# Kernel optimization log

Hardware: AMD Instinct MI355X
Metric: run time of the kernel (lower is better)

The kernel has to match this reference:

```python
import jax, jax.numpy as jnp
import numpy as np

B, S, D = 2, 2048, 1024
H, HD = 16, 64          # num_heads, head_dim = D // H
W = 31                  # window_size (odd)
E = 1024                # embed_dim


def setup_inputs() -> dict:
    key = jax.random.key(0)
    ks = jax.random.split(key, 12)
    sd = 1.0 / np.sqrt(D)
    so = 1.0 / np.sqrt(H * HD)
    return {
        "x": jax.random.normal(ks[0], (B, S, D), jnp.float32),
        "fsq": jax.random.normal(ks[1], (1, S, D), jnp.float32),   # feature_squeeze_token
        "pos": jax.random.normal(ks[2], (1, S, D), jnp.float32),   # position_token
        "Wq": jax.random.normal(ks[3], (H, D, HD), jnp.float32) * sd,
        "bq": jax.random.normal(ks[4], (H, HD), jnp.float32) * sd,
        "Wk": jax.random.normal(ks[5], (H, D, HD), jnp.float32) * sd,
        "bk": jax.random.normal(ks[6], (H, HD), jnp.float32) * sd,
        "Wv": jax.random.normal(ks[7], (H, D, HD), jnp.float32) * sd,
        "bv": jax.random.normal(ks[8], (H, HD), jnp.float32) * sd,
        "Wo": jax.random.normal(ks[9], (H * HD, E), jnp.float32) * so,
        "bo": jax.random.normal(ks[10], (E,), jnp.float32) * so,
    }


def reference(x, fsq, pos, Wq, bq, Wk, bk, Wv, bv, Wo, bo):
    b, s, d = x.shape
    pad = (W - 1) // 2
    # sliding windows: (B, S, W, D), zero-padded at sequence edges
    xp = jnp.pad(x, ((0, 0), (pad, pad), (0, 0)))
    idx = jnp.arange(s)[:, None] + jnp.arange(W)[None, :]  # (S, W)
    win = xp[:, idx, :]  # (B, S, W, D)
    a = jnp.broadcast_to(fsq[:, :, None, :], (b, s, 1, d))  # squeeze token per pos
    bt = jnp.broadcast_to(pos[:, :, None, :], (b, s, 1, d))  # position token per pos
    kv = jnp.concatenate([win, bt, a], axis=2)  # (B, S, K=W+2, D)
    q = jnp.broadcast_to(fsq, (b, s, d))        # query = squeeze token
    # per-head projections (heads stacked on axis h)
    qh = jnp.einsum("bsd,hde->bhse", q, Wq) + bq[None, :, None, :]        # (B,H,S,HD)
    kh = jnp.einsum("bskd,hde->bhske", kv, Wk) + bk[None, :, None, None, :]
    vh = jnp.einsum("bskd,hde->bhske", kv, Wv) + bv[None, :, None, None, :]
    scores = jnp.einsum("bhse,bhske->bhsk", qh, kh) / jnp.sqrt(jnp.asarray(HD, x.dtype))
    attn = jax.nn.softmax(scores, axis=-1)  # dropout is identity in eval
    outh = jnp.einsum("bhsk,bhske->bhse", attn, vh)  # (B,H,S,HD)
    concat = outh.transpose(0, 2, 1, 3).reshape(b, s, H * HD)  # heads concat order 0..H-1
    return concat @ Wo + bo  # (B, S, E)
```

## Files before the change

### kernel.cpp

```cpp
#include <hip/hip_runtime.h>


typedef __attribute__((ext_vector_type(8))) short bf16x8;
typedef __attribute__((ext_vector_type(4))) float f32x4;
typedef unsigned short u16;
typedef unsigned int u32;
typedef unsigned long long u64;

__device__ __forceinline__ float bf2f(u16 u) {
  union { u32 i; float f; } v; v.i = ((u32)u) << 16; return v.f;
}
__device__ __forceinline__ u16 f2bf(float f) {
  union { float f; u32 i; } v; v.f = f;
  u32 r = v.i + 0x7fffu + ((v.i >> 16) & 1u);
  return (u16)(r >> 16);
}
__device__ __forceinline__ float2 unpk(u32 u) {
  union { u32 i; float f; } lo, hi;
  lo.i = u << 16; hi.i = u & 0xffff0000u;
  return make_float2(lo.f, hi.f);
}
__device__ __forceinline__ float dot8(uint4 a, uint4 b) {
  float s = 0.f;
  { float2 x = unpk(a.x), y = unpk(b.x); s += x.x*y.x + x.y*y.y; }
  { float2 x = unpk(a.y), y = unpk(b.y); s += x.x*y.x + x.y*y.y; }
  { float2 x = unpk(a.z), y = unpk(b.z); s += x.x*y.x + x.y*y.y; }
  { float2 x = unpk(a.w), y = unpk(b.w); s += x.x*y.x + x.y*y.y; }
  return s;
}
__device__ __forceinline__ void gload_lds16(const u16* g, u16* l) {
  __builtin_amdgcn_global_load_lds((const __attribute__((address_space(1))) void*)(g),
                                   (__attribute__((address_space(3))) void*)(l),
                                   16, 0, 0);
}
__device__ __forceinline__ uint4 pack8(float4 a, float4 b) {
  union { u16 h[8]; uint4 q; } u;
  u.h[0] = f2bf(a.x); u.h[1] = f2bf(a.y); u.h[2] = f2bf(a.z); u.h[3] = f2bf(a.w);
  u.h[4] = f2bf(b.x); u.h[5] = f2bf(b.y); u.h[6] = f2bf(b.z); u.h[7] = f2bf(b.w);
  return u.q;
}

__device__ __forceinline__ void transpose_body(const float* src, u16* dst,
                                               int R, int C, int r0, int c0) {
  __shared__ u16 tile[64][72];
  int t = threadIdx.x;
#pragma unroll
  for (int i = 0; i < 16; ++i) {
    int idx = i * 256 + t;
    int r = idx >> 6, c = idx & 63;
    tile[r][c] = f2bf(src[(size_t)(r0 + r) * C + (c0 + c)]);
  }
  __syncthreads();
#pragma unroll
  for (int i = 0; i < 16; ++i) {
    int idx = i * 256 + t;
    int c = idx >> 6, r = idx & 63;
    dst[(size_t)(c0 + c) * R + (r0 + r)] = tile[r][c];
  }
}

__global__ __launch_bounds__(256) void prep(const float* __restrict__ x,
                                            const float* __restrict__ fsq,
                                            const float* __restrict__ pos,
                                            const float* __restrict__ Wq,
                                            const float* __restrict__ Wk,
                                            const float* __restrict__ Wv,
                                            const float* __restrict__ Wo,
                                            u16* __restrict__ xb,
                                            u16* __restrict__ fsqb,
                                            u16* __restrict__ posb,
                                            u16* __restrict__ WqT,
                                            u16* __restrict__ WkT,
                                            u16* __restrict__ WvT,
                                            u16* __restrict__ WoT) {
  int bid = blockIdx.x;
  if (bid < 4096) {
    int i = bid * 256 + threadIdx.x;
    const float* src; u16* dst; int off;
    if (i < 524288)      { src = x;   dst = xb;   off = i; }
    else if (i < 786432) { src = fsq; dst = fsqb; off = i - 524288; }
    else                 { src = pos; dst = posb; off = i - 786432; }
    float4 a = ((const float4*)src)[2 * off];
    float4 b = ((const float4*)src)[2 * off + 1];
    ((uint4*)dst)[off] = pack8(a, b);
  } else {
    int id = bid - 4096;
    int z = id >> 8, rest = id & 255;
    int xx = rest & 15, yy = rest >> 4;
    if (z < 3) {
      const float* s = (z == 0) ? Wq : (z == 1) ? Wk : Wv;
      u16* d = (z == 0) ? WqT : (z == 1) ? WkT : WvT;
      size_t off = (size_t)xx * 65536;
      transpose_body(s + off, d + off, 1024, 64, yy * 64, 0);
    } else {
      transpose_body(Wo, WoT, 1024, 1024, yy * 64, xx * 64);
    }
  }
}

__device__ __forceinline__ int swz(int R, int c) {
  return (R * 8 + (c ^ (R & 7))) * 8;
}

__global__ __launch_bounds__(512) void proj_gemm(const u16* __restrict__ xb,
                                                 const u16* __restrict__ fsqb,
                                                 const u16* __restrict__ posb,
                                                 const u16* __restrict__ WkT,
                                                 const u16* __restrict__ WvT,
                                                 const u16* __restrict__ WqT,
                                                 const float* __restrict__ bk,
                                                 const float* __restrict__ bv,
                                                 const float* __restrict__ bq,
                                                 u16* __restrict__ Kp,
                                                 u16* __restrict__ VpT,
                                                 u16* __restrict__ Vd,
                                                 u16* __restrict__ Qp) {
  __shared__ u16 As[128 * 64];
  __shared__ u16 Bs[256 * 64];

  const int bid = blockIdx.x;
  const int t = threadIdx.x, lane = t & 63, wave = t >> 6;
  const int row16 = lane & 15, quad = lane >> 4;
  const int l8 = lane >> 3;
  const int cswz = (lane & 7) ^ l8;

  const u16 *Ap, *BTa, *BTb;
  const float *biasA, *biasB;
  u16 *C1, *C2rm;
  int c1_noff, c2_noff;
  bool c2_t = false;
  int tmb = 0;

  if (bid < 512) {
    int tm = bid >> 3, tn = bid & 7;
    if (tm < 32)      Ap = xb   + (size_t)tm * 131072;
    else if (tm < 48) Ap = fsqb + (size_t)(tm - 32) * 131072;
    else              Ap = posb + (size_t)(tm - 48) * 131072;
    BTa = WkT + (size_t)(tn * 128) * 1024;
    BTb = WvT + (size_t)(tn * 128) * 1024;
    biasA = bk; biasB = bv;
    C1 = Kp + (size_t)tm * 131072; c1_noff = tn * 128;
    c2_noff = tn * 128;
    if (tm < 32) { c2_t = true; tmb = tm * 128; C2rm = nullptr; }
    else         { C2rm = Vd + (size_t)(tm - 32) * 131072; }
  } else {
    int q = bid - 512;
    int tm = q >> 2, tn4 = q & 3;
    Ap  = fsqb + (size_t)tm * 131072;
    BTa = WqT + (size_t)(tn4 * 256) * 1024;
    BTb = WqT + (size_t)(tn4 * 256 + 128) * 1024;
    biasA = bq; biasB = bq;
    C1 = Qp + (size_t)tm * 131072;  c1_noff = tn4 * 256;
    C2rm = C1;                      c2_noff = tn4 * 256 + 128;
  }

  const int wm = (wave >> 2) * 64, wn = (wave & 3) * 64;
  f32x4 acc[4][4] = {};

  for (int k0 = 0; k0 < 1024; k0 += 64) {
    __syncthreads();
#pragma unroll
    for (int j = 0; j < 2; ++j) {
      int r = wave * 16 + j * 8 + l8;
      gload_lds16(Ap + (size_t)r * 1024 + k0 + cswz * 8,
                  &As[wave * 1024 + j * 512]);
    }
    const u16* Bsrc = (wave < 4) ? BTa : BTb;
    const int rb = (wave & 3) * 32;
#pragma unroll
    for (int j = 0; j < 4; ++j) {
      int r = rb + j * 8 + l8;
      gload_lds16(Bsrc + (size_t)r * 1024 + k0 + cswz * 8,
                  &Bs[wave * 2048 + j * 512]);
    }
    __syncthreads();

#pragma unroll
    for (int kb = 0; kb < 2; ++kb) {
      bf16x8 a_frag[4], b_frag[4];
#pragma unroll
      for (int i = 0; i < 4; ++i)
        a_frag[i] = *(const bf16x8*)&As[swz(wm + i * 16 + row16, kb * 4 + quad)];
#pragma unroll
      for (int j = 0; j < 4; ++j)
        b_frag[j] = *(const bf16x8*)&Bs[swz(wn + j * 16 + row16, kb * 4 + quad)];
#pragma unroll
      for (int i = 0; i < 4; ++i)
#pragma unroll
        for (int j = 0; j < 4; ++j)
          acc[i][j] = __builtin_amdgcn_mfma_f32_16x16x32_bf16(
              a_frag[i], b_frag[j], acc[i][j], 0, 0, 0);
    }
  }

  if (wn < 128) {
#pragma unroll
    for (int j = 0; j < 4; ++j) {
      int n = c1_noff + wn + j * 16 + row16;
      float bb = biasA[n];
#pragma unroll
      for (int i = 0; i < 4; ++i) {
        int m0 = wm + i * 16 + quad * 4;
#pragma unroll
        for (int r = 0; r < 4; ++r)
          C1[(size_t)(m0 + r) * 1024 + n] = f2bf(acc[i][j][r] + bb);
      }
    }
  } else if (c2_t) {
#pragma unroll
    for (int j = 0; j < 4; ++j) {
      int nv = c2_noff + (wn - 128) + j * 16 + row16;
      float bb = biasB[nv];
#pragma unroll
      for (int i = 0; i < 4; ++i) {
        int m0 = wm + i * 16 + quad * 4;
        union { u16 h[4]; u64 q; } o;
#pragma unroll
        for (int r = 0; r < 4; ++r) o.h[r] = f2bf(acc[i][j][r] + bb);
        *(u64*)(VpT + (size_t)nv * 4096 + tmb + m0) = o.q;
      }
    }
  } else {
#pragma unroll
    for (int j = 0; j < 4; ++j) {
      int nv = c2_noff + (wn - 128) + j * 16 + row16;
      float bb = biasB[nv];
#pragma unroll
      for (int i = 0; i < 4; ++i) {
        int m0 = wm + i * 16 + quad * 4;
#pragma unroll
        for (int r = 0; r < 4; ++r)
          C2rm[(size_t)(m0 + r) * 1024 + nv] = f2bf(acc[i][j][r] + bb);
      }
    }
  }
}

__global__ __launch_bounds__(256) void out_gemm(const u16* __restrict__ Att,
                                                const u16* __restrict__ WoT,
                                                const float* __restrict__ bo,
                                                float* __restrict__ Out) {
  __shared__ u16 As[64 * 128];
  __shared__ u16 Bs[128 * 128];
  const int tile_n = blockIdx.x * 128, tm = blockIdx.y;
  const u16* Ap = Att + (size_t)tm * 65536;
  float* Cp = Out + (size_t)tm * 65536;

  const int t = threadIdx.x, lane = t & 63, wave = t >> 6;
  const int wm = (wave >> 1) * 32, wn = (wave & 1) * 64;
  const int row16 = lane & 15, quad = lane >> 4;

  f32x4 acc[2][4] = {};

  for (int k0 = 0; k0 < 1024; k0 += 128) {
    __syncthreads();
#pragma unroll
    for (int j = 0; j < 4; ++j) {
      int idx = wave * 256 + j * 64 + lane;
      int r = idx >> 4, c = (idx & 15) ^ (r & 15);
      gload_lds16(Ap + (size_t)r * 1024 + k0 + c * 8,
                  &As[wave * 2048 + j * 512]);
    }
#pragma unroll
    for (int j = 0; j < 8; ++j) {
      int idx = wave * 512 + j * 64 + lane;
      int r = idx >> 4, c = (idx & 15) ^ (r & 15);
      gload_lds16(WoT + (size_t)(tile_n + r) * 1024 + k0 + c * 8,
                  &Bs[wave * 4096 + j * 512]);
    }
    __syncthreads();

#pragma unroll
    for (int kb = 0; kb < 4; ++kb) {
      bf16x8 a_frag[2], b_frag[4];
#pragma unroll
      for (int i = 0; i < 2; ++i) {
        int R = wm + i * 16 + row16, c = kb * 4 + quad;
        a_frag[i] = *(const bf16x8*)&As[(R * 16 + (c ^ (R & 15))) * 8];
      }
#pragma unroll
      for (int j = 0; j < 4; ++j) {
        int R = wn + j * 16 + row16, c = kb * 4 + quad;
        b_frag[j] = *(const bf16x8*)&Bs[(R * 16 + (c ^ (R & 15))) * 8];
      }
#pragma unroll
      for (int i = 0; i < 2; ++i)
#pragma unroll
        for (int j = 0; j < 4; ++j)
          acc[i][j] = __builtin_amdgcn_mfma_f32_16x16x32_bf16(
              a_frag[i], b_frag[j], acc[i][j], 0, 0, 0);
    }
  }

#pragma unroll
  for (int j = 0; j < 4; ++j) {
    int n = tile_n + wn + j * 16 + row16;
    float bb = bo[n];
#pragma unroll
    for (int i = 0; i < 2; ++i) {
      int m0 = wm + i * 16 + quad * 4;
#pragma unroll
      for (int r = 0; r < 4; ++r)
        Cp[(size_t)(m0 + r) * 1024 + n] = acc[i][j][r] + bb;
    }
  }
}

#define QS   0
#define KPS  2304
#define KFS  4608
#define KWS  6912
#define VTS  11008
#define SMT  15104

__global__ __launch_bounds__(256) void attn_tile(const u16* __restrict__ Qp,
                                                 const u16* __restrict__ Kp,
                                                 const u16* __restrict__ VpT,
                                                 const u16* __restrict__ Vd,
                                                 const float* __restrict__ bk,
                                                 const float* __restrict__ bv,
                                                 u16* __restrict__ Att) {
  __shared__ u16 sm[SMT];
  __shared__ float smP[32 * 36];

  const int t = threadIdx.x;
  const int bid = blockIdx.x;
  const int s0 = (bid & 63) * 32;
  const int h  = (bid >> 6) & 15;
  const int b  = bid >> 10;
  const int lane = t & 63, wave = t >> 6;
  const int row16 = lane & 15, quad = lane >> 4;
  const int hcol = h * 64;

  { int w = t >> 3, oct = t & 7;
    *(uint4*)&sm[QS + w * 72 + oct * 8] =
        *(const uint4*)(Qp + (size_t)(s0 + w) * 1024 + hcol + oct * 8); }
  { int r = t >> 3, oct = t & 7;
    *(uint4*)&sm[KPS + r * 72 + oct * 8] =
        *(const uint4*)(Kp + (size_t)(6144 + s0 + r) * 1024 + hcol + oct * 8);
    *(uint4*)&sm[KFS + r * 72 + oct * 8] =
        *(const uint4*)(Kp + (size_t)(4096 + s0 + r) * 1024 + hcol + oct * 8); }

  const bool boundary = (s0 == 0) || (s0 == 2016);
  if (!boundary) {
#pragma unroll
    for (int i = 0; i < 2; ++i) {
      int task = i * 256 + t;
      int w = task >> 3, oct = task & 7;
      gload_lds16(Kp + (size_t)(b * 2048 + s0 + w - 16) * 1024 + hcol + oct * 8,
                  &sm[KWS + (i * 256 + wave * 64) * 8]);
      int e = w;
      gload_lds16(VpT + (size_t)(hcol + e) * 4096 + (b * 2048 + s0 - 16) + oct * 8,
                  &sm[VTS + (i * 256 + wave * 64) * 8]);
    }
  } else {
#pragma unroll
    for (int i = 0; i < 2; ++i) {
      int task = i * 256 + t;
      int w = task >> 3, oct = task & 7;
      int g = s0 + w - 16;
      uint4 kv;
      if ((unsigned)g < 2048u)
        kv = *(const uint4*)(Kp + (size_t)(b * 2048 + g) * 1024 + hcol + oct * 8);
      else
        kv = pack8(*(const float4*)(bk + hcol + oct * 8),
                   *(const float4*)(bk + hcol + oct * 8 + 4));
      *(uint4*)&sm[KWS + w * 64 + oct * 8] = kv;

      int e = w;
      int g0 = s0 + oct * 8 - 16;
      uint4 vv;
      if (g0 >= 0 && g0 + 7 < 2048)
        vv = *(const uint4*)(VpT + (size_t)(hcol + e) * 4096 + (b * 2048 + g0));
      else {
        u16 hb = f2bf(bv[hcol + e]);
        u32 pp = (u32)hb | ((u32)hb << 16);
        vv = make_uint4(pp, pp, pp, pp);
      }
      *(uint4*)&sm[VTS + e * 64 + oct * 8] = vv;
    }
  }
  __syncthreads();

  {
    f32x4 accS[2] = {};
#pragma unroll
    for (int kc = 0; kc < 2; ++kc) {
      bf16x8 bf_ = *(const bf16x8*)&sm[KWS + (wave * 16 + row16) * 64 + kc * 32 + quad * 8];
#pragma unroll
      for (int mi = 0; mi < 2; ++mi) {
        bf16x8 af = *(const bf16x8*)&sm[QS + (mi * 16 + row16) * 72 + kc * 32 + quad * 8];
        accS[mi] = __builtin_amdgcn_mfma_f32_16x16x32_bf16(af, bf_, accS[mi], 0, 0, 0);
      }
    }
#pragma unroll
    for (int mi = 0; mi < 2; ++mi)
#pragma unroll
      for (int r = 0; r < 4; ++r) {
        int s = mi * 16 + quad * 4 + r;
        int w = wave * 16 + row16;
        int d = w - s;
        if (d >= 1 && d <= 31) smP[s * 36 + d - 1] = accS[mi][r] * 0.125f;
      }
  }
  if (t < 64) {
    int s = t >> 1, which = t & 1;
    int base = (which == 0) ? KPS : KFS;
    float a = 0.f;
#pragma unroll
    for (int c = 0; c < 8; ++c)
      a += dot8(*(const uint4*)&sm[QS + s * 72 + c * 8],
                *(const uint4*)&sm[base + s * 72 + c * 8]);
    smP[s * 36 + 31 + which] = a * 0.125f;
  }
  __syncthreads();

  if (t < 64) {
    const int s = t >> 1, half = t & 1;
    const int kb_ = half * 17;
    float vals[17];
#pragma unroll
    for (int k = 0; k < 17; ++k) {
      int kk = kb_ + k;
      vals[k] = (kk < 33) ? smP[s * 36 + kk] : -1e30f;
    }
    float mx = -1e30f;
#pragma unroll
    for (int k = 0; k < 17; ++k) mx = fmaxf(mx, vals[k]);
    mx = fmaxf(mx, __shfl_xor(mx, 1, 64));
    float sum = 0.f;
#pragma unroll
    for (int k = 0; k < 17; ++k) { vals[k] = __expf(vals[k] - mx); sum += vals[k]; }
    sum += __shfl_xor(sum, 1, 64);
    const float inv = 1.f / sum;
    u32* prow = (u32*)&sm[QS + s * 72];
#pragma unroll
    for (int j = 0; j < 16; ++j) prow[half * 16 + j] = 0;
#pragma unroll
    for (int k = 0; k < 17; ++k) {
      int kk = kb_ + k;
      if (kk < 31)      sm[QS + s * 72 + (s + 1 + kk)] = f2bf(vals[k] * inv);
      else if (kk < 33) smP[s * 36 + 2 + kk] = vals[k] * inv;
    }
  }
  __syncthreads();

  {
    f32x4 accO[2] = {};
#pragma unroll
    for (int kc = 0; kc < 2; ++kc) {
      bf16x8 bf_ = *(const bf16x8*)&sm[VTS + (wave * 16 + row16) * 64 + kc * 32 + quad * 8];
#pragma unroll
      for (int mi = 0; mi < 2; ++mi) {
        bf16x8 af = *(const bf16x8*)&sm[QS + (mi * 16 + row16) * 72 + kc * 32 + quad * 8];
        accO[mi] = __builtin_amdgcn_mfma_f32_16x16x32_bf16(af, bf_, accO[mi], 0, 0, 0);
      }
    }
#pragma unroll
    for (int mi = 0; mi < 2; ++mi)
#pragma unroll
      for (int r = 0; r < 4; ++r) {
        int s = mi * 16 + quad * 4 + r;
        int e = wave * 16 + row16;
        float o = accO[mi][r]
                + smP[s * 36 + 33] * bf2f(Vd[(size_t)(2048 + s0 + s) * 1024 + hcol + e])
                + smP[s * 36 + 34] * bf2f(Vd[(size_t)(s0 + s) * 1024 + hcol + e]);
        Att[(size_t)(b * 2048 + s0 + s) * 1024 + hcol + e] = f2bf(o);
      }
  }
}

extern "C" void kernel_launch(void* const* d_in, const int* in_sizes, int n_in,
                              void* d_out, int out_size, void* d_ws, size_t ws_size,
                              hipStream_t stream) {
  (void)in_sizes; (void)n_in; (void)out_size; (void)ws_size;

  const float* x   = (const float*)d_in[0];
  const float* fsq = (const float*)d_in[1];
  const float* pos = (const float*)d_in[2];
  const float* Wq  = (const float*)d_in[3];
  const float* bq  = (const float*)d_in[4];
  const float* Wk  = (const float*)d_in[5];
  const float* bk  = (const float*)d_in[6];
  const float* Wv  = (const float*)d_in[7];
  const float* bv  = (const float*)d_in[8];
  const float* Wo  = (const float*)d_in[9];
  const float* bo  = (const float*)d_in[10];

  u16* ws = (u16*)d_ws;
  const size_t M1 = 1024 * 1024;
  u16* WqT  = ws + 0 * M1;
  u16* WkT  = ws + 1 * M1;
  u16* WvT  = ws + 2 * M1;
  u16* WoT  = ws + 3 * M1;
  u16* Qp   = ws + 4 * M1;
  u16* Kp   = ws + 6 * M1;
  u16* VpT  = ws + 14 * M1;
  u16* Vd   = ws + 18 * M1;
  u16* fsqb = ws + 22 * M1;
  u16* posb = ws + 24 * M1;
  u16* xb   = ws + 26 * M1;
  u16* Att  = ws + 22 * M1;

  prep<<<5120, 256, 0, stream>>>(x, fsq, pos, Wq, Wk, Wv, Wo,
                                 xb, fsqb, posb, WqT, WkT, WvT, WoT);

  proj_gemm<<<576, 512, 0, stream>>>(xb, fsqb, posb, WkT, WvT, WqT,
                                     bk, bv, bq, Kp, VpT, Vd, Qp);

  attn_tile<<<2048, 256, 0, stream>>>(Qp, Kp, VpT, Vd, bk, bv, Att);

  out_gemm<<<dim3(8, 64), 256, 0, stream>>>(Att, WoT, bo, (float*)d_out);
}
```

Before: 199.4 us.

## Shrink projection GEMM tiles to 128x128 and remap block IDs for XCD locality

The projection GEMM moves from 512-thread blocks computing a 128x256 tile to 256-thread blocks computing 128x128 tiles, doubling the grid to 1152 blocks and halving B-tile shared memory. Block IDs in both the projection and output GEMMs are permuted so that consecutive hardware-dispatched blocks (round-robin across the eight XCDs) land on the same logical row group, improving L2 reuse of the A operand. The intent is better occupancy, load balance and cache locality, at the cost of reloading A tiles twice as often per output column range.

```diff
diff --git a/kernel.cpp b/kernel.cpp
--- a/kernel.cpp
+++ b/kernel.cpp
@@ -102,7 +102,7 @@
   return (R * 8 + (c ^ (R & 7))) * 8;
 }
 
-__global__ __launch_bounds__(512) void proj_gemm(const u16* __restrict__ xb,
+__global__ __launch_bounds__(256) void proj_gemm(const u16* __restrict__ xb,
                                                  const u16* __restrict__ fsqb,
                                                  const u16* __restrict__ posb,
                                                  const u16* __restrict__ WkT,
@@ -116,61 +116,63 @@
                                                  u16* __restrict__ Vd,
                                                  u16* __restrict__ Qp) {
   __shared__ u16 As[128 * 64];
-  __shared__ u16 Bs[256 * 64];
+  __shared__ u16 Bs[128 * 64];
 
   const int bid = blockIdx.x;
+  const int lb = (bid & 7) * 144 + (bid >> 3);
   const int t = threadIdx.x, lane = t & 63, wave = t >> 6;
   const int row16 = lane & 15, quad = lane >> 4;
   const int l8 = lane >> 3;
   const int cswz = (lane & 7) ^ l8;
 
-  const u16 *Ap, *BTa, *BTb;
-  const float *biasA, *biasB;
-  u16 *C1, *C2rm;
-  int c1_noff, c2_noff;
-  bool c2_t = false;
-  int tmb = 0;
-
-  if (bid < 512) {
-    int tm = bid >> 3, tn = bid & 7;
+  const u16 *Ap, *BT;
+  const float* bias;
+  u16* Crm = nullptr;
+  u16* Cvt = nullptr;
+  int noff = 0, tmb = 0;
+
+  if (lb < 1024) {
+    int tm = lb >> 4, tn = lb & 15;
     if (tm < 32)      Ap = xb   + (size_t)tm * 131072;
     else if (tm < 48) Ap = fsqb + (size_t)(tm - 32) * 131072;
     else              Ap = posb + (size_t)(tm - 48) * 131072;
-    BTa = WkT + (size_t)(tn * 128) * 1024;
-    BTb = WvT + (size_t)(tn * 128) * 1024;
-    biasA = bk; biasB = bv;
-    C1 = Kp + (size_t)tm * 131072; c1_noff = tn * 128;
-    c2_noff = tn * 128;
-    if (tm < 32) { c2_t = true; tmb = tm * 128; C2rm = nullptr; }
-    else         { C2rm = Vd + (size_t)(tm - 32) * 131072; }
+    if (tn < 8) {
+      BT = WkT + (size_t)(tn * 128) * 1024;
+      bias = bk;
+      Crm = Kp + (size_t)tm * 131072;
+      noff = tn * 128;
+    } else {
+      BT = WvT + (size_t)((tn - 8) * 128) * 1024;
+      bias = bv;
+      noff = (tn - 8) * 128;
+      if (tm < 32) { Cvt = VpT; tmb = tm * 128; }
+      else         { Crm = Vd + (size_t)(tm - 32) * 131072; }
+    }
   } else {
-    int q = bid - 512;
-    int tm = q >> 2, tn4 = q & 3;
-    Ap  = fsqb + (size_t)tm * 131072;
-    BTa = WqT + (size_t)(tn4 * 256) * 1024;
-    BTb = WqT + (size_t)(tn4 * 256 + 128) * 1024;
-    biasA = bq; biasB = bq;
-    C1 = Qp + (size_t)tm * 131072;  c1_noff = tn4 * 256;
-    C2rm = C1;                      c2_noff = tn4 * 256 + 128;
-  }
-
-  const int wm = (wave >> 2) * 64, wn = (wave & 3) * 64;
+    int q2 = lb - 1024;
+    int tm = q2 >> 3, tn = q2 & 7;
+    Ap = fsqb + (size_t)tm * 131072;
+    BT = WqT + (size_t)(tn * 128) * 1024;
+    bias = bq;
+    Crm = Qp + (size_t)tm * 131072;
+    noff = tn * 128;
+  }
+
+  const int wm = (wave >> 1) * 64, wn = (wave & 1) * 64;
   f32x4 acc[4][4] = {};
 
   for (int k0 = 0; k0 < 1024; k0 += 64) {
     __syncthreads();
 #pragma unroll
-    for (int j = 0; j < 2; ++j) {
-      int r = wave * 16 + j * 8 + l8;
+    for (int j = 0; j < 4; ++j) {
+      int r = wave * 32 + j * 8 + l8;
       gload_lds16(Ap + (size_t)r * 1024 + k0 + cswz * 8,
-                  &As[wave * 1024 + j * 512]);
-    }
-    const u16* Bsrc = (wave < 4) ? BTa : BTb;
-    const int rb = (wave & 3) * 32;
+                  &As[wave * 2048 + j * 512]);
+    }
 #pragma unroll
     for (int j = 0; j < 4; ++j) {
-      int r = rb + j * 8 + l8;
-      gload_lds16(Bsrc + (size_t)r * 1024 + k0 + cswz * 8,
+      int r = wave * 32 + j * 8 + l8;
+      gload_lds16(BT + (size_t)r * 1024 + k0 + cswz * 8,
                   &Bs[wave * 2048 + j * 512]);
     }
     __syncthreads();
@@ -193,44 +195,31 @@
     }
   }
 
-  if (wn < 128) {
+  if (Cvt) {
 #pragma unroll
     for (int j = 0; j < 4; ++j) {
-      int n = c1_noff + wn + j * 16 + row16;
-      float bb = biasA[n];
-#pragma unroll
-      for (int i = 0; i < 4; ++i) {
-        int m0 = wm + i * 16 + quad * 4;
-#pragma unroll
-        for (int r = 0; r < 4; ++r)
-          C1[(size_t)(m0 + r) * 1024 + n] = f2bf(acc[i][j][r] + bb);
-      }
-    }
-  } else if (c2_t) {
-#pragma unroll
-    for (int j = 0; j < 4; ++j) {
-      int nv = c2_noff + (wn - 128) + j * 16 + row16;
-      float bb = biasB[nv];
+      int nv = noff + wn + j * 16 + row16;
+      float bb = bias[nv];
 #pragma unroll
       for (int i = 0; i < 4; ++i) {
         int m0 = wm + i * 16 + quad * 4;
         union { u16 h[4]; u64 q; } o;
 #pragma unroll
         for (int r = 0; r < 4; ++r) o.h[r] = f2bf(acc[i][j][r] + bb);
-        *(u64*)(VpT + (size_t)nv * 4096 + tmb + m0) = o.q;
+        *(u64*)(Cvt + (size_t)nv * 4096 + tmb + m0) = o.q;
       }
     }
   } else {
 #pragma unroll
     for (int j = 0; j < 4; ++j) {
-      int nv = c2_noff + (wn - 128) + j * 16 + row16;
-      float bb = biasB[nv];
+      int n = noff + wn + j * 16 + row16;
+      float bb = bias[n];
 #pragma unroll
       for (int i = 0; i < 4; ++i) {
         int m0 = wm + i * 16 + quad * 4;
 #pragma unroll
         for (int r = 0; r < 4; ++r)
-          C2rm[(size_t)(m0 + r) * 1024 + nv] = f2bf(acc[i][j][r] + bb);
+          Crm[(size_t)(m0 + r) * 1024 + n] = f2bf(acc[i][j][r] + bb);
       }
     }
   }
@@ -242,7 +231,10 @@
                                                 float* __restrict__ Out) {
   __shared__ u16 As[64 * 128];
   __shared__ u16 Bs[128 * 128];
-  const int tile_n = blockIdx.x * 128, tm = blockIdx.y;
+  const int bid = blockIdx.x;
+  const int lb = (bid & 7) * 64 + (bid >> 3);
+  const int tile_n = (lb & 7) * 128;
+  const int tm = lb >> 3;
   const u16* Ap = Att + (size_t)tm * 65536;
   float* Cp = Out + (size_t)tm * 65536;
 
@@ -505,10 +497,10 @@
   prep<<<5120, 256, 0, stream>>>(x, fsq, pos, Wq, Wk, Wv, Wo,
                                  xb, fsqb, posb, WqT, WkT, WvT, WoT);
 
-  proj_gemm<<<576, 512, 0, stream>>>(xb, fsqb, posb, WkT, WvT, WqT,
-                                     bk, bv, bq, Kp, VpT, Vd, Qp);
+  proj_gemm<<<1152, 256, 0, stream>>>(xb, fsqb, posb, WkT, WvT, WqT,
+                                      bk, bv, bq, Kp, VpT, Vd, Qp);
 
   attn_tile<<<2048, 256, 0, stream>>>(Qp, Kp, VpT, Vd, bk, bv, Att);
 
-  out_gemm<<<dim3(8, 64), 256, 0, stream>>>(Att, WoT, bo, (float*)d_out);
-}
+  out_gemm<<<512, 256, 0, stream>>>(Att, WoT, bo, (float*)d_out);
+}
```

Result: no change. 200.5 us (+0.6%).

## Double-buffer LDS tiles and remap block order in projection and output GEMMs

Applied to the files above, without the earlier changes.

Both GEMM kernels move to a two-stage LDS ping-pong: the next K tile is issued as a direct global-to-LDS load while MFMAs run on the current tile, which drops one barrier per iteration. Block indices are also remapped so consecutive hardware blocks spread across tile columns and XCDs, aiming for better L2 reuse of the weight and activation tiles. The cost is doubled LDS (96KB for proj_gemm), which may lower occupancy. The prefetch also relies on the buffer-load completing before the end-of-iteration barrier.

```diff
diff --git a/kernel.cpp b/kernel.cpp
--- a/kernel.cpp
+++ b/kernel.cpp
@@ -115,10 +115,11 @@
                                                  u16* __restrict__ VpT,
                                                  u16* __restrict__ Vd,
                                                  u16* __restrict__ Qp) {
-  __shared__ u16 As[128 * 64];
-  __shared__ u16 Bs[256 * 64];
+  __shared__ u16 As[2][128 * 64];
+  __shared__ u16 Bs[2][256 * 64];
 
   const int bid = blockIdx.x;
+  const int lb = (bid & 7) * 72 + (bid >> 3);
   const int t = threadIdx.x, lane = t & 63, wave = t >> 6;
   const int row16 = lane & 15, quad = lane >> 4;
   const int l8 = lane >> 3;
@@ -131,8 +132,8 @@
   bool c2_t = false;
   int tmb = 0;
 
-  if (bid < 512) {
-    int tm = bid >> 3, tn = bid & 7;
+  if (lb < 512) {
+    int tm = lb >> 3, tn = lb & 7;
     if (tm < 32)      Ap = xb   + (size_t)tm * 131072;
     else if (tm < 48) Ap = fsqb + (size_t)(tm - 32) * 131072;
     else              Ap = posb + (size_t)(tm - 48) * 131072;
@@ -144,7 +145,7 @@
     if (tm < 32) { c2_t = true; tmb = tm * 128; C2rm = nullptr; }
     else         { C2rm = Vd + (size_t)(tm - 32) * 131072; }
   } else {
-    int q = bid - 512;
+    int q = lb - 512;
     int tm = q >> 2, tn4 = q & 3;
     Ap  = fsqb + (size_t)tm * 131072;
     BTa = WqT + (size_t)(tn4 * 256) * 1024;
@@ -157,33 +158,40 @@
   const int wm = (wave >> 2) * 64, wn = (wave & 3) * 64;
   f32x4 acc[4][4] = {};
 
-  for (int k0 = 0; k0 < 1024; k0 += 64) {
-    __syncthreads();
+  const u16* Bsrc = (wave < 4) ? BTa : BTb;
+  const int rb = (wave & 3) * 32;
+
+  auto stage = [&](int buf, int k0) {
 #pragma unroll
     for (int j = 0; j < 2; ++j) {
       int r = wave * 16 + j * 8 + l8;
       gload_lds16(Ap + (size_t)r * 1024 + k0 + cswz * 8,
-                  &As[wave * 1024 + j * 512]);
-    }
-    const u16* Bsrc = (wave < 4) ? BTa : BTb;
-    const int rb = (wave & 3) * 32;
+                  &As[buf][wave * 1024 + j * 512]);
+    }
 #pragma unroll
     for (int j = 0; j < 4; ++j) {
       int r = rb + j * 8 + l8;
       gload_lds16(Bsrc + (size_t)r * 1024 + k0 + cswz * 8,
-                  &Bs[wave * 2048 + j * 512]);
-    }
-    __syncthreads();
+                  &Bs[buf][wave * 2048 + j * 512]);
+    }
+  };
+
+  stage(0, 0);
+  __syncthreads();
+  int cur = 0;
+
+  for (int kt = 0; kt < 16; ++kt) {
+    if (kt < 15) stage(cur ^ 1, (kt + 1) * 64);
 
 #pragma unroll
     for (int kb = 0; kb < 2; ++kb) {
       bf16x8 a_frag[4], b_frag[4];
 #pragma unroll
       for (int i = 0; i < 4; ++i)
-        a_frag[i] = *(const bf16x8*)&As[swz(wm + i * 16 + row16, kb * 4 + quad)];
+        a_frag[i] = *(const bf16x8*)&As[cur][swz(wm + i * 16 + row16, kb * 4 + quad)];
 #pragma unroll
       for (int j = 0; j < 4; ++j)
-        b_frag[j] = *(const bf16x8*)&Bs[swz(wn + j * 16 + row16, kb * 4 + quad)];
+        b_frag[j] = *(const bf16x8*)&Bs[cur][swz(wn + j * 16 + row16, kb * 4 + quad)];
 #pragma unroll
       for (int i = 0; i < 4; ++i)
 #pragma unroll
@@ -191,6 +199,9 @@
           acc[i][j] = __builtin_amdgcn_mfma_f32_16x16x32_bf16(
               a_frag[i], b_frag[j], acc[i][j], 0, 0, 0);
     }
+
+    __syncthreads();
+    cur ^= 1;
   }
 
   if (wn < 128) {
@@ -240,9 +251,12 @@
                                                 const u16* __restrict__ WoT,
                                                 const float* __restrict__ bo,
                                                 float* __restrict__ Out) {
-  __shared__ u16 As[64 * 128];
-  __shared__ u16 Bs[128 * 128];
-  const int tile_n = blockIdx.x * 128, tm = blockIdx.y;
+  __shared__ u16 As[2][64 * 128];
+  __shared__ u16 Bs[2][128 * 128];
+  const int bid = blockIdx.x;
+  const int lb = (bid & 7) * 64 + (bid >> 3);
+  const int tile_n = (lb & 7) * 128;
+  const int tm = lb >> 3;
   const u16* Ap = Att + (size_t)tm * 65536;
   float* Cp = Out + (size_t)tm * 65536;
 
@@ -252,23 +266,29 @@
 
   f32x4 acc[2][4] = {};
 
-  for (int k0 = 0; k0 < 1024; k0 += 128) {
-    __syncthreads();
+  auto stage = [&](int buf, int k0) {
 #pragma unroll
     for (int j = 0; j < 4; ++j) {
       int idx = wave * 256 + j * 64 + lane;
       int r = idx >> 4, c = (idx & 15) ^ (r & 15);
       gload_lds16(Ap + (size_t)r * 1024 + k0 + c * 8,
-                  &As[wave * 2048 + j * 512]);
+                  &As[buf][wave * 2048 + j * 512]);
     }
 #pragma unroll
     for (int j = 0; j < 8; ++j) {
       int idx = wave * 512 + j * 64 + lane;
       int r = idx >> 4, c = (idx & 15) ^ (r & 15);
       gload_lds16(WoT + (size_t)(tile_n + r) * 1024 + k0 + c * 8,
-                  &Bs[wave * 4096 + j * 512]);
-    }
-    __syncthreads();
+                  &Bs[buf][wave * 4096 + j * 512]);
+    }
+  };
+
+  stage(0, 0);
+  __syncthreads();
+  int cur = 0;
+
+  for (int kt = 0; kt < 8; ++kt) {
+    if (kt < 7) stage(cur ^ 1, (kt + 1) * 128);
 
 #pragma unroll
     for (int kb = 0; kb < 4; ++kb) {
@@ -276,12 +296,12 @@
 #pragma unroll
       for (int i = 0; i < 2; ++i) {
         int R = wm + i * 16 + row16, c = kb * 4 + quad;
-        a_frag[i] = *(const bf16x8*)&As[(R * 16 + (c ^ (R & 15))) * 8];
+        a_frag[i] = *(const bf16x8*)&As[cur][(R * 16 + (c ^ (R & 15))) * 8];
       }
 #pragma unroll
       for (int j = 0; j < 4; ++j) {
         int R = wn + j * 16 + row16, c = kb * 4 + quad;
-        b_frag[j] = *(const bf16x8*)&Bs[(R * 16 + (c ^ (R & 15))) * 8];
+        b_frag[j] = *(const bf16x8*)&Bs[cur][(R * 16 + (c ^ (R & 15))) * 8];
       }
 #pragma unroll
       for (int i = 0; i < 2; ++i)
@@ -290,6 +310,9 @@
           acc[i][j] = __builtin_amdgcn_mfma_f32_16x16x32_bf16(
               a_frag[i], b_frag[j], acc[i][j], 0, 0, 0);
     }
+
+    __syncthreads();
+    cur ^= 1;
   }
 
 #pragma unroll
@@ -510,5 +533,5 @@
 
   attn_tile<<<2048, 256, 0, stream>>>(Qp, Kp, VpT, Vd, bk, bv, Att);
 
-  out_gemm<<<dim3(8, 64), 256, 0, stream>>>(Att, WoT, bo, (float*)d_out);
-}
+  out_gemm<<<512, 256, 0, stream>>>(Att, WoT, bo, (float*)d_out);
+}
```

After: 225.9 us. 1.13x slower.
